# Kernel optimization log

Hardware: AMD Instinct MI355X
Metric: run time of the kernel (lower is better)

Reference implementation:

```python
import jax, jax.numpy as jnp
import numpy as np

N = 100000
E = 1600000
IN_DIM = 128
HID = 64
EPS = 1e-5


def setup_inputs() -> dict:
    key = jax.random.key(0)
    ks = jax.random.split(key, 16)
    x = jax.random.normal(ks[0], (N, IN_DIM), dtype=jnp.float32)
    edge_index = jax.random.randint(ks[1], (2, E), 0, N, dtype=jnp.int32)
    def glorot(k, fan_in, fan_out):
        s = jnp.sqrt(6.0 / (fan_in + fan_out))
        return jax.random.uniform(k, (fan_in, fan_out), jnp.float32, -s, s)
    return {
        "x": x,
        "edge_index": edge_index,
        "W0": glorot(ks[2], IN_DIM, HID), "b0": jnp.zeros((HID,), jnp.float32),
        "W1": glorot(ks[3], HID, HID),    "b1": jnp.zeros((HID,), jnp.float32),
        "W2": glorot(ks[4], HID, HID),    "b2": jnp.zeros((HID,), jnp.float32),
        "g0": jnp.ones((HID,), jnp.float32),  "be0": jnp.zeros((HID,), jnp.float32),
        "g1": jnp.ones((HID,), jnp.float32),  "be1": jnp.zeros((HID,), jnp.float32),
        "g2": jnp.ones((HID,), jnp.float32),  "be2": jnp.zeros((HID,), jnp.float32),
        "fc1_w": glorot(ks[5], HID, 32), "fc1_b": jnp.zeros((32,), jnp.float32),
        "fc2_w": glorot(ks[6], 32, 2),   "fc2_b": jnp.zeros((2,), jnp.float32),
    }


def _gcn_conv(x, src, dst, dis, W, b):
    # x' = D^{-1/2} (A + I) D^{-1/2} (x W) + b ; dis = deg^{-1/2} with self-loops
    h = x @ W                                   # [N, H]
    norm = dis[src] * dis[dst]                  # [E]
    msg = h[src] * norm[:, None]                # [E, H]
    agg = jax.ops.segment_sum(msg, dst, num_segments=N)
    agg = agg + h * (dis * dis)[:, None]        # self-loop contribution
    return agg + b


def _batchnorm(x, gamma, beta):
    mu = jnp.mean(x, axis=0)
    var = jnp.mean(jnp.square(x - mu), axis=0)  # biased, as torch BN training
    return gamma * (x - mu) * jax.lax.rsqrt(var + EPS) + beta


def reference(x, edge_index, W0, b0, W1, b1, W2, b2,
              g0, be0, g1, be1, g2, be2, fc1_w, fc1_b, fc2_w, fc2_b):
    src = edge_index[0]
    dst = edge_index[1]
    deg = jax.ops.segment_sum(jnp.ones((E,), x.dtype), dst, num_segments=N) + 1.0
    dis = jax.lax.rsqrt(deg)                    # deg >= 1 from self-loops
    for W, b, g, be in ((W0, b0, g0, be0), (W1, b1, g1, be1), (W2, b2, g2, be2)):
        x = _gcn_conv(x, src, dst, dis, W, b)
        x = jax.nn.relu(_batchnorm(x, g, be))
        # dropout: identity (deterministic eval)
    x = jax.nn.relu(x @ fc1_w + fc1_b)
    x = x @ fc2_w + fc2_b
    return jax.nn.log_softmax(x, axis=1)
```

## Files before the change

### kernel.cpp

```cpp
#include <hip/hip_runtime.h>
#include <hip/hip_fp16.h>
#include <math.h>


#define BUCK_CAP 6144
#define PB_EDGES 8192

typedef _Float16 f16x8 __attribute__((ext_vector_type(8)));
typedef float f32x4 __attribute__((ext_vector_type(4)));

union H4U { uint2 u; __half h[4]; };
union H8U { uint4 u; __half h[8]; };

__device__ inline uint2 pack4(float a, float b, float c, float d) {
    H4U t;
    t.h[0] = __float2half_rn(a); t.h[1] = __float2half_rn(b);
    t.h[2] = __float2half_rn(c); t.h[3] = __float2half_rn(d);
    return t.u;
}
__device__ inline float4 unpack4(uint2 u) {
    H4U t; t.u = u;
    return make_float4(__half2float(t.h[0]), __half2float(t.h[1]),
                       __half2float(t.h[2]), __half2float(t.h[3]));
}
__device__ inline void upadd8(uint4 u, float* a) {
    H8U t; t.u = u;
#pragma unroll
    for (int i = 0; i < 8; ++i) a[i] += __half2float(t.h[i]);
}

__global__ __launch_bounds__(256) void k_zero(int* __restrict__ gcur,
                                              float* __restrict__ stats) {
    int t = threadIdx.x;
    gcur[t] = 0; gcur[t + 256] = 0;
    stats[t] = 0.f;
    if (t < 128) stats[256 + t] = 0.f;
}

__global__ __launch_bounds__(256) void k_part(const int* __restrict__ src,
                                              const int* __restrict__ dst,
                                              int* __restrict__ gcur,
                                              unsigned* __restrict__ rec,
                                              int E, int NB) {
    __shared__ int hist[512];
    __shared__ int lbase[512];
    __shared__ int gbase[512];
    __shared__ int stmp[256];
    __shared__ unsigned stage[PB_EDGES];
    __shared__ unsigned short sbkt[PB_EDGES];
    const int tid = threadIdx.x;
    const int e0 = blockIdx.x * PB_EDGES;
    const int e1 = min(e0 + PB_EDGES, E);
    const int cnt = e1 - e0;

    hist[tid] = 0; hist[tid + 256] = 0;
    __syncthreads();
    for (int i = e0 + tid; i < e1; i += 256)
        atomicAdd(&hist[dst[i] >> 8], 1);
    __syncthreads();
    for (int b = tid; b < NB; b += 256) {
        int c = hist[b];
        gbase[b] = c ? atomicAdd(&gcur[b], c) : 0;
    }
    int h0 = hist[2 * tid], h1 = hist[2 * tid + 1];
    int psum = h0 + h1;
    stmp[tid] = psum;
    __syncthreads();
    int x = psum;
    for (int off = 1; off < 256; off <<= 1) {
        int y = (tid >= off) ? stmp[tid - off] : 0;
        __syncthreads();
        x += y;
        stmp[tid] = x;
        __syncthreads();
    }
    int excl = x - psum;
    lbase[2 * tid] = excl;
    lbase[2 * tid + 1] = excl + h0;
    __syncthreads();
    hist[2 * tid] = excl;
    hist[2 * tid + 1] = excl + h0;
    __syncthreads();
    for (int i = e0 + tid; i < e1; i += 256) {
        int s = src[i], d = dst[i];
        int b = d >> 8;
        int pos = atomicAdd(&hist[b], 1);
        stage[pos] = ((unsigned)s << 8) | (unsigned)(d & 255);
        sbkt[pos] = (unsigned short)b;
    }
    __syncthreads();
    for (int i = tid; i < cnt; i += 256) {
        int b = sbkt[i];
        rec[(size_t)b * BUCK_CAP + gbase[b] + (i - lbase[b])] = stage[i];
    }
}

__global__ __launch_bounds__(256) void k_bscat(const int* __restrict__ gcur,
                                               const unsigned* __restrict__ rec,
                                               float* __restrict__ dis,
                                               int* __restrict__ row_ptr,
                                               int* __restrict__ ssrc,
                                               int n, int NB, int E) {
    __shared__ int h[256];
    __shared__ int cur[256];
    __shared__ int lb[512];
    __shared__ int stmp[256];
    __shared__ int stage[BUCK_CAP];
    const int b = blockIdx.x, tid = threadIdx.x;
    int g0 = (2 * tid < NB) ? gcur[2 * tid] : 0;
    int g1 = (2 * tid + 1 < NB) ? gcur[2 * tid + 1] : 0;
    int ps = g0 + g1;
    stmp[tid] = ps;
    h[tid] = 0;
    __syncthreads();
    int xx = ps;
    for (int off = 1; off < 256; off <<= 1) {
        int y = (tid >= off) ? stmp[tid - off] : 0;
        __syncthreads();
        xx += y;
        stmp[tid] = xx;
        __syncthreads();
    }
    int ex = xx - ps;
    lb[2 * tid] = ex;
    lb[2 * tid + 1] = ex + g0;
    __syncthreads();
    const int bb = lb[b];
    if (b == 0 && tid == 0) row_ptr[n] = E;

    const int cnt = gcur[b];
    const unsigned* r = rec + (size_t)b * BUCK_CAP;
    for (int i = tid; i < cnt; i += 256)
        atomicAdd(&h[r[i] & 255u], 1);
    __syncthreads();
    const int myd = h[tid];
    const int node = b * 256 + tid;
    if (node < n) dis[node] = rsqrtf((float)myd + 1.0f);
    int x = myd;
    for (int off = 1; off < 256; off <<= 1) {
        int y = (tid >= off) ? h[tid - off] : 0;
        __syncthreads();
        x += y;
        h[tid] = x;
        __syncthreads();
    }
    const int excl = x - myd;
    if (node < n) row_ptr[node] = bb + excl;
    cur[tid] = excl;
    __syncthreads();
    for (int i = tid; i < cnt; i += 256) {
        unsigned v = r[i];
        int pos = atomicAdd(&cur[v & 255u], 1);
        stage[pos] = (int)(v >> 8);
    }
    __syncthreads();
    for (int i = tid; i < cnt; i += 256) ssrc[bb + i] = stage[i];
}

template <int K, bool BN, bool XH>
__global__ __launch_bounds__(256) void k_gemm(const void* __restrict__ Xv,
                                              const float* __restrict__ W,
                                              const float* __restrict__ dis,
                                              const float* __restrict__ stats,
                                              const float* __restrict__ g,
                                              const float* __restrict__ be,
                                              __half* __restrict__ Hp, int n) {
    constexpr int KS = K / 32;
    constexpr int XSTR = K + 8;
    __shared__ __align__(16) __half BF[KS * 4 * 64 * 8];
    __shared__ __align__(16) __half XL[64 * XSTR];
    __shared__ float muS[64], wS[64], bS[64];
    const int tid = threadIdx.x;
    const int row0 = blockIdx.x * 64;

    if constexpr (BN) {
        if (tid < 64) {
            float inv_n = 1.0f / (float)n;
            float m = stats[tid] * inv_n;
            float var = stats[64 + tid] * inv_n - m * m;
            muS[tid] = m;
            wS[tid] = rsqrtf(var + 1e-5f) * g[tid];
            bS[tid] = be[tid];
        }
    }
    for (int i = tid; i < KS * 4 * 64; i += 256) {
        int l = i & 63, fs = i >> 6;
        int ks = fs >> 2, ct = fs & 3;
        int kb = ks * 32 + ((l >> 4) << 3);
        int c = (ct << 4) + (l & 15);
        H8U t;
#pragma unroll
        for (int j = 0; j < 8; ++j) t.h[j] = __float2half_rn(W[(kb + j) * 64 + c]);
        *reinterpret_cast<uint4*>(&BF[i * 8]) = t.u;
    }
    __syncthreads();

    if constexpr (!XH) {
        constexpr int Q4 = K / 4;
        const float4* X4 = (const float4*)Xv;
        for (int it = 0; it < 64 * Q4 / 256; ++it) {
            int idx = it * 256 + tid;
            int row = idx / Q4, q = idx % Q4;
            int grow = row0 + row;
            float4 v = make_float4(0.f, 0.f, 0.f, 0.f);
            if (grow < n) v = X4[(size_t)grow * Q4 + q];
            *reinterpret_cast<uint2*>(&XL[row * XSTR + q * 4]) = pack4(v.x, v.y, v.z, v.w);
        }
    } else {
        constexpr int QU = K / 4;
        const uint2* Xh = (const uint2*)Xv;
        for (int it = 0; it < 64 * QU / 256; ++it) {
            int idx = it * 256 + tid;
            int row = idx / QU, q = idx % QU;
            int grow = row0 + row;
            float4 v = make_float4(0.f, 0.f, 0.f, 0.f);
            if (grow < n) {
                v = unpack4(Xh[(size_t)grow * QU + q]);
                float4 m = *reinterpret_cast<const float4*>(&muS[q * 4]);
                float4 w4 = *reinterpret_cast<const float4*>(&wS[q * 4]);
                float4 b4 = *reinterpret_cast<const float4*>(&bS[q * 4]);
                v.x = fmaxf((v.x - m.x) * w4.x + b4.x, 0.f);
                v.y = fmaxf((v.y - m.y) * w4.y + b4.y, 0.f);
                v.z = fmaxf((v.z - m.z) * w4.z + b4.z, 0.f);
                v.w = fmaxf((v.w - m.w) * w4.w + b4.w, 0.f);
            }
            *reinterpret_cast<uint2*>(&XL[row * XSTR + q * 4]) = pack4(v.x, v.y, v.z, v.w);
        }
    }
    __syncthreads();

    const int wave = tid >> 6, lane = tid & 63;
    const __half* arow = &XL[(wave * 16 + (lane & 15)) * XSTR + ((lane >> 4) << 3)];
    f16x8 a[KS];
#pragma unroll
    for (int ks = 0; ks < KS; ++ks)
        a[ks] = *reinterpret_cast<const f16x8*>(arow + ks * 32);

    f32x4 acc[4];
#pragma unroll
    for (int ct = 0; ct < 4; ++ct) acc[ct] = (f32x4){0.f, 0.f, 0.f, 0.f};
#pragma unroll
    for (int ct = 0; ct < 4; ++ct)
#pragma unroll
        for (int ks = 0; ks < KS; ++ks) {
            f16x8 b = *reinterpret_cast<const f16x8*>(&BF[((ks * 4 + ct) * 64 + lane) * 8]);
            acc[ct] = __builtin_amdgcn_mfma_f32_16x16x32_f16(a[ks], b, acc[ct], 0, 0, 0);
        }

    const int mbase = row0 + wave * 16 + ((lane >> 4) << 2);
#pragma unroll
    for (int reg = 0; reg < 4; ++reg) {
        int grow = mbase + reg;
        if (grow < n) {
            float dd = dis[grow];
#pragma unroll
            for (int ct = 0; ct < 4; ++ct)
                Hp[(size_t)grow * 64 + ct * 16 + (lane & 15)] =
                    __float2half_rn(acc[ct][reg] * dd);
        }
    }
}

__global__ __launch_bounds__(256) void k_gather(const int* __restrict__ row_ptr,
                                                const int* __restrict__ ssrc,
                                                const float* __restrict__ dis,
                                                const uint4* __restrict__ Hp,
                                                uint4* __restrict__ AGG, int n) {
    int t = blockIdx.x * 256 + threadIdx.x;
    int d = t >> 3;
    if (d >= n) return;
    int fi = t & 7;
    int r0 = row_ptr[d], r1 = row_ptr[d + 1];
    float a[8] = {};
    upadd8(Hp[(size_t)d * 8 + fi], a);
    int p = r0;
    for (; p + 7 < r1; p += 8) {
        int s0 = ssrc[p], s1 = ssrc[p + 1], s2 = ssrc[p + 2], s3 = ssrc[p + 3];
        int s4 = ssrc[p + 4], s5 = ssrc[p + 5], s6 = ssrc[p + 6], s7 = ssrc[p + 7];
        uint4 q0 = Hp[(size_t)s0 * 8 + fi];
        uint4 q1 = Hp[(size_t)s1 * 8 + fi];
        uint4 q2 = Hp[(size_t)s2 * 8 + fi];
        uint4 q3 = Hp[(size_t)s3 * 8 + fi];
        uint4 q4 = Hp[(size_t)s4 * 8 + fi];
        uint4 q5 = Hp[(size_t)s5 * 8 + fi];
        uint4 q6 = Hp[(size_t)s6 * 8 + fi];
        uint4 q7 = Hp[(size_t)s7 * 8 + fi];
        upadd8(q0, a); upadd8(q1, a); upadd8(q2, a); upadd8(q3, a);
        upadd8(q4, a); upadd8(q5, a); upadd8(q6, a); upadd8(q7, a);
    }
    for (; p + 3 < r1; p += 4) {
        int s0 = ssrc[p], s1 = ssrc[p + 1], s2 = ssrc[p + 2], s3 = ssrc[p + 3];
        uint4 q0 = Hp[(size_t)s0 * 8 + fi];
        uint4 q1 = Hp[(size_t)s1 * 8 + fi];
        uint4 q2 = Hp[(size_t)s2 * 8 + fi];
        uint4 q3 = Hp[(size_t)s3 * 8 + fi];
        upadd8(q0, a); upadd8(q1, a); upadd8(q2, a); upadd8(q3, a);
    }
    for (; p < r1; ++p) upadd8(Hp[(size_t)ssrc[p] * 8 + fi], a);
    float dd = dis[d];
    H8U o;
#pragma unroll
    for (int i = 0; i < 8; ++i) o.h[i] = __float2half_rn(a[i] * dd);
    AGG[(size_t)d * 8 + fi] = o.u;
}

__global__ __launch_bounds__(256) void k_stats(const uint2* __restrict__ A,
                                               float* __restrict__ stats, int n) {
    __shared__ float r1[16 * 64];
    __shared__ float r2[16 * 64];
    int tid = threadIdx.x;
    int fi = tid & 15, rg = tid >> 4;
    float s0 = 0, s1 = 0, s2 = 0, s3 = 0, q0 = 0, q1 = 0, q2 = 0, q3 = 0;
    for (int row = blockIdx.x * 16 + rg; row < n; row += gridDim.x * 16) {
        float4 v = unpack4(A[(size_t)row * 16 + fi]);
        s0 += v.x; q0 += v.x * v.x;
        s1 += v.y; q1 += v.y * v.y;
        s2 += v.z; q2 += v.z * v.z;
        s3 += v.w; q3 += v.w * v.w;
    }
    r1[rg * 64 + fi * 4 + 0] = s0; r2[rg * 64 + fi * 4 + 0] = q0;
    r1[rg * 64 + fi * 4 + 1] = s1; r2[rg * 64 + fi * 4 + 1] = q1;
    r1[rg * 64 + fi * 4 + 2] = s2; r2[rg * 64 + fi * 4 + 2] = q2;
    r1[rg * 64 + fi * 4 + 3] = s3; r2[rg * 64 + fi * 4 + 3] = q3;
    __syncthreads();
    if (tid < 64) {
        float a = 0;
#pragma unroll
        for (int r = 0; r < 16; ++r) a += r1[r * 64 + tid];
        atomicAdd(&stats[tid], a);
    } else if (tid < 128) {
        int f = tid - 64;
        float a = 0;
#pragma unroll
        for (int r = 0; r < 16; ++r) a += r2[r * 64 + f];
        atomicAdd(&stats[64 + f], a);
    }
}

__global__ __launch_bounds__(256) void k_head(const uint2* __restrict__ X,
                                              const float* __restrict__ stats,
                                              const float* __restrict__ g,
                                              const float* __restrict__ be,
                                              const float* __restrict__ w1,
                                              const float* __restrict__ b1,
                                              const float* __restrict__ w2,
                                              const float* __restrict__ b2,
                                              float* __restrict__ out, int n) {
    __shared__ __align__(16) float w1s[64 * 32];
    __shared__ __align__(16) float b1s[32];
    __shared__ float w2s[64];
    __shared__ float b2s[2];
    __shared__ float muS[64], wS[64], bS[64];
    int tid = threadIdx.x;
    for (int i = tid; i < 512; i += 256)
        reinterpret_cast<float4*>(w1s)[i] = reinterpret_cast<const float4*>(w1)[i];
    if (tid < 32) b1s[tid] = b1[tid];
    if (tid >= 64 && tid < 128) w2s[tid - 64] = w2[tid - 64];
    if (tid >= 128 && tid < 130) b2s[tid - 128] = b2[tid - 128];
    if (tid < 64) {
        float inv_n = 1.0f / (float)n;
        float m = stats[tid] * inv_n;
        float var = stats[64 + tid] * inv_n - m * m;
        muS[tid] = m;
        wS[tid] = rsqrtf(var + 1e-5f) * g[tid];
        bS[tid] = be[tid];
    }
    __syncthreads();
    int row = blockIdx.x * 256 + tid;
    if (row >= n) return;

    float4 h[8];
#pragma unroll
    for (int j4 = 0; j4 < 8; ++j4) h[j4] = reinterpret_cast<float4*>(b1s)[j4];

#pragma unroll
    for (int k4 = 0; k4 < 16; ++k4) {
        float4 xv = unpack4(X[(size_t)row * 16 + k4]);
#pragma unroll
        for (int kk = 0; kk < 4; ++kk) {
            int k = k4 * 4 + kk;
            float raw = (kk == 0) ? xv.x : (kk == 1) ? xv.y : (kk == 2) ? xv.z : xv.w;
            float xk = fmaxf((raw - muS[k]) * wS[k] + bS[k], 0.f);
            const float4* wrow = reinterpret_cast<const float4*>(&w1s[k * 32]);
#pragma unroll
            for (int j4 = 0; j4 < 8; ++j4) {
                float4 wv = wrow[j4];
                h[j4].x += xk * wv.x; h[j4].y += xk * wv.y;
                h[j4].z += xk * wv.z; h[j4].w += xk * wv.w;
            }
        }
    }
    float o0 = b2s[0], o1 = b2s[1];
#pragma unroll
    for (int j4 = 0; j4 < 8; ++j4) {
        float hv[4] = {h[j4].x, h[j4].y, h[j4].z, h[j4].w};
#pragma unroll
        for (int c = 0; c < 4; ++c) {
            float hj = fmaxf(hv[c], 0.f);
            int j = j4 * 4 + c;
            o0 += hj * w2s[2 * j];
            o1 += hj * w2s[2 * j + 1];
        }
    }
    float m = fmaxf(o0, o1);
    float l = __logf(__expf(o0 - m) + __expf(o1 - m));
    reinterpret_cast<float2*>(out)[row] = make_float2(o0 - m - l, o1 - m - l);
}

extern "C" void kernel_launch(void* const* d_in, const int* in_sizes, int n_in,
                              void* d_out, int out_size, void* d_ws, size_t ws_size,
                              hipStream_t stream) {
    const float* x    = (const float*)d_in[0];
    const int*   ei   = (const int*)d_in[1];
    const float* W0   = (const float*)d_in[2];
    const float* W1   = (const float*)d_in[4];
    const float* W2   = (const float*)d_in[6];
    const float* g0   = (const float*)d_in[8];
    const float* be0  = (const float*)d_in[9];
    const float* g1   = (const float*)d_in[10];
    const float* be1  = (const float*)d_in[11];
    const float* g2   = (const float*)d_in[12];
    const float* be2  = (const float*)d_in[13];
    const float* fc1w = (const float*)d_in[14];
    const float* fc1b = (const float*)d_in[15];
    const float* fc2w = (const float*)d_in[16];
    const float* fc2b = (const float*)d_in[17];

    const int N = in_sizes[0] / 128;
    const int E = in_sizes[1] / 2;
    const int* srcp = ei;
    const int* dstp = ei + E;
    const int NB = (N + 255) >> 8;

    char* ws = (char*)d_ws;
    size_t off = 0;
    auto alloc = [&](size_t bytes) -> void* {
        void* p = ws + off;
        off = (off + bytes + 255) & ~(size_t)255;
        return p;
    };
    int*      gcur    = (int*)alloc(512 * 4);
    float*    stats   = (float*)alloc(3 * 128 * 4);
    float*    dis     = (float*)alloc((size_t)N * 4);
    int*      row_ptr = (int*)alloc((size_t)(N + 1) * 4);
    unsigned* rec     = (unsigned*)alloc((size_t)NB * BUCK_CAP * 4);
    int*      ssrc    = (int*)alloc((size_t)E * 4);
    __half*   B0      = (__half*)alloc((size_t)N * 64 * 2);
    __half*   B1      = (__half*)alloc((size_t)N * 64 * 2);

    k_zero<<<1, 256, 0, stream>>>(gcur, stats);
    k_part<<<(E + PB_EDGES - 1) / PB_EDGES, 256, 0, stream>>>(srcp, dstp, gcur, rec, E, NB);
    k_bscat<<<NB, 256, 0, stream>>>(gcur, rec, dis, row_ptr, ssrc, N, NB, E);

    const int gemm_grid = (N + 63) / 64;
    const int gath_grid = (N * 8 + 255) / 256;

    k_gemm<128, false, false><<<gemm_grid, 256, 0, stream>>>(x, W0, dis, nullptr, nullptr, nullptr, B0, N);
    k_gather<<<gath_grid, 256, 0, stream>>>(row_ptr, ssrc, dis, (const uint4*)B0, (uint4*)B1, N);
    k_stats<<<512, 256, 0, stream>>>((const uint2*)B1, stats + 0, N);

    k_gemm<64, true, true><<<gemm_grid, 256, 0, stream>>>(B1, W1, dis, stats + 0, g0, be0, B0, N);
    k_gather<<<gath_grid, 256, 0, stream>>>(row_ptr, ssrc, dis, (const uint4*)B0, (uint4*)B1, N);
    k_stats<<<512, 256, 0, stream>>>((const uint2*)B1, stats + 128, N);

    k_gemm<64, true, true><<<gemm_grid, 256, 0, stream>>>(B1, W2, dis, stats + 128, g1, be1, B0, N);
    k_gather<<<gath_grid, 256, 0, stream>>>(row_ptr, ssrc, dis, (const uint4*)B0, (uint4*)B1, N);
    k_stats<<<512, 256, 0, stream>>>((const uint2*)B1, stats + 256, N);

    k_head<<<(N + 255) / 256, 256, 0, stream>>>((const uint2*)B1, stats + 256, g2, be2,
                                                fc1w, fc1b, fc2w, fc2b,
                                                (float*)d_out, N);
}
```

Baseline: 253.3 us.

## Fuse BatchNorm statistics into gather kernel with striped atomic accumulators

Folds the per-feature sum and sum-of-squares reduction into the gather kernel, which now runs as a fixed grid-stride launch. This drops the separate stats kernel and its re-read of the aggregated half-precision buffer. The stats are computed from fp32 values before fp16 rounding and accumulated into 8 striped slots chosen by block index, which the consumers then sum, to cut atomic contention. The fixed grid of 2048 blocks may lower parallelism and latency hiding in the gather compared with the previous one-thread-per-feature-chunk launch.

```diff
diff --git a/kernel.cpp b/kernel.cpp
--- a/kernel.cpp
+++ b/kernel.cpp
@@ -5,6 +5,7 @@
 
 #define BUCK_CAP 6144
 #define PB_EDGES 8192
+#define GATH_BLOCKS 2048
 
 typedef _Float16 f16x8 __attribute__((ext_vector_type(8)));
 typedef float f32x4 __attribute__((ext_vector_type(4)));
@@ -33,8 +34,8 @@
                                               float* __restrict__ stats) {
     int t = threadIdx.x;
     gcur[t] = 0; gcur[t + 256] = 0;
-    stats[t] = 0.f;
-    if (t < 128) stats[256 + t] = 0.f;
+#pragma unroll
+    for (int k = 0; k < 12; ++k) stats[k * 256 + t] = 0.f;
 }
 
 __global__ __launch_bounds__(256) void k_part(const int* __restrict__ src,
@@ -175,9 +176,15 @@
 
     if constexpr (BN) {
         if (tid < 64) {
+            float s1 = 0.f, s2 = 0.f;
+#pragma unroll
+            for (int r = 0; r < 8; ++r) {
+                s1 += stats[r * 128 + tid];
+                s2 += stats[r * 128 + 64 + tid];
+            }
             float inv_n = 1.0f / (float)n;
-            float m = stats[tid] * inv_n;
-            float var = stats[64 + tid] * inv_n - m * m;
+            float m = s1 * inv_n;
+            float var = s2 * inv_n - m * m;
             muS[tid] = m;
             wS[tid] = rsqrtf(var + 1e-5f) * g[tid];
             bS[tid] = be[tid];
@@ -265,75 +272,69 @@
                                                 const int* __restrict__ ssrc,
                                                 const float* __restrict__ dis,
                                                 const uint4* __restrict__ Hp,
-                                                uint4* __restrict__ AGG, int n) {
-    int t = blockIdx.x * 256 + threadIdx.x;
-    int d = t >> 3;
-    if (d >= n) return;
-    int fi = t & 7;
-    int r0 = row_ptr[d], r1 = row_ptr[d + 1];
-    float a[8] = {};
-    upadd8(Hp[(size_t)d * 8 + fi], a);
-    int p = r0;
-    for (; p + 7 < r1; p += 8) {
-        int s0 = ssrc[p], s1 = ssrc[p + 1], s2 = ssrc[p + 2], s3 = ssrc[p + 3];
-        int s4 = ssrc[p + 4], s5 = ssrc[p + 5], s6 = ssrc[p + 6], s7 = ssrc[p + 7];
-        uint4 q0 = Hp[(size_t)s0 * 8 + fi];
-        uint4 q1 = Hp[(size_t)s1 * 8 + fi];
-        uint4 q2 = Hp[(size_t)s2 * 8 + fi];
-        uint4 q3 = Hp[(size_t)s3 * 8 + fi];
-        uint4 q4 = Hp[(size_t)s4 * 8 + fi];
-        uint4 q5 = Hp[(size_t)s5 * 8 + fi];
-        uint4 q6 = Hp[(size_t)s6 * 8 + fi];
-        uint4 q7 = Hp[(size_t)s7 * 8 + fi];
-        upadd8(q0, a); upadd8(q1, a); upadd8(q2, a); upadd8(q3, a);
-        upadd8(q4, a); upadd8(q5, a); upadd8(q6, a); upadd8(q7, a);
-    }
-    for (; p + 3 < r1; p += 4) {
-        int s0 = ssrc[p], s1 = ssrc[p + 1], s2 = ssrc[p + 2], s3 = ssrc[p + 3];
-        uint4 q0 = Hp[(size_t)s0 * 8 + fi];
-        uint4 q1 = Hp[(size_t)s1 * 8 + fi];
-        uint4 q2 = Hp[(size_t)s2 * 8 + fi];
-        uint4 q3 = Hp[(size_t)s3 * 8 + fi];
-        upadd8(q0, a); upadd8(q1, a); upadd8(q2, a); upadd8(q3, a);
-    }
-    for (; p < r1; ++p) upadd8(Hp[(size_t)ssrc[p] * 8 + fi], a);
-    float dd = dis[d];
-    H8U o;
-#pragma unroll
-    for (int i = 0; i < 8; ++i) o.h[i] = __float2half_rn(a[i] * dd);
-    AGG[(size_t)d * 8 + fi] = o.u;
-}
-
-__global__ __launch_bounds__(256) void k_stats(const uint2* __restrict__ A,
-                                               float* __restrict__ stats, int n) {
-    __shared__ float r1[16 * 64];
-    __shared__ float r2[16 * 64];
-    int tid = threadIdx.x;
-    int fi = tid & 15, rg = tid >> 4;
-    float s0 = 0, s1 = 0, s2 = 0, s3 = 0, q0 = 0, q1 = 0, q2 = 0, q3 = 0;
-    for (int row = blockIdx.x * 16 + rg; row < n; row += gridDim.x * 16) {
-        float4 v = unpack4(A[(size_t)row * 16 + fi]);
-        s0 += v.x; q0 += v.x * v.x;
-        s1 += v.y; q1 += v.y * v.y;
-        s2 += v.z; q2 += v.z * v.z;
-        s3 += v.w; q3 += v.w * v.w;
-    }
-    r1[rg * 64 + fi * 4 + 0] = s0; r2[rg * 64 + fi * 4 + 0] = q0;
-    r1[rg * 64 + fi * 4 + 1] = s1; r2[rg * 64 + fi * 4 + 1] = q1;
-    r1[rg * 64 + fi * 4 + 2] = s2; r2[rg * 64 + fi * 4 + 2] = q2;
-    r1[rg * 64 + fi * 4 + 3] = s3; r2[rg * 64 + fi * 4 + 3] = q3;
+                                                uint4* __restrict__ AGG,
+                                                float* __restrict__ stats, int n) {
+    __shared__ float red[32][64];
+    const int tid = threadIdx.x;
+    const int g = tid >> 3, fi = tid & 7;
+    float sacc[8] = {}, qacc[8] = {};
+    for (int d = blockIdx.x * 32 + g; d < n; d += gridDim.x * 32) {
+        int r0 = row_ptr[d], r1 = row_ptr[d + 1];
+        float a[8] = {};
+        upadd8(Hp[(size_t)d * 8 + fi], a);
+        int p = r0;
+        for (; p + 7 < r1; p += 8) {
+            int s0 = ssrc[p], s1 = ssrc[p + 1], s2 = ssrc[p + 2], s3 = ssrc[p + 3];
+            int s4 = ssrc[p + 4], s5 = ssrc[p + 5], s6 = ssrc[p + 6], s7 = ssrc[p + 7];
+            uint4 q0 = Hp[(size_t)s0 * 8 + fi];
+            uint4 q1 = Hp[(size_t)s1 * 8 + fi];
+            uint4 q2 = Hp[(size_t)s2 * 8 + fi];
+            uint4 q3 = Hp[(size_t)s3 * 8 + fi];
+            uint4 q4 = Hp[(size_t)s4 * 8 + fi];
+            uint4 q5 = Hp[(size_t)s5 * 8 + fi];
+            uint4 q6 = Hp[(size_t)s6 * 8 + fi];
+            uint4 q7 = Hp[(size_t)s7 * 8 + fi];
+            upadd8(q0, a); upadd8(q1, a); upadd8(q2, a); upadd8(q3, a);
+            upadd8(q4, a); upadd8(q5, a); upadd8(q6, a); upadd8(q7, a);
+        }
+        for (; p + 3 < r1; p += 4) {
+            int s0 = ssrc[p], s1 = ssrc[p + 1], s2 = ssrc[p + 2], s3 = ssrc[p + 3];
+            uint4 q0 = Hp[(size_t)s0 * 8 + fi];
+            uint4 q1 = Hp[(size_t)s1 * 8 + fi];
+            uint4 q2 = Hp[(size_t)s2 * 8 + fi];
+            uint4 q3 = Hp[(size_t)s3 * 8 + fi];
+            upadd8(q0, a); upadd8(q1, a); upadd8(q2, a); upadd8(q3, a);
+        }
+        for (; p < r1; ++p) upadd8(Hp[(size_t)ssrc[p] * 8 + fi], a);
+        float dd = dis[d];
+        H8U o;
+#pragma unroll
+        for (int i = 0; i < 8; ++i) {
+            float v = a[i] * dd;
+            o.h[i] = __float2half_rn(v);
+            sacc[i] += v;
+            qacc[i] += v * v;
+        }
+        AGG[(size_t)d * 8 + fi] = o.u;
+    }
+#pragma unroll
+    for (int j = 0; j < 8; ++j) red[g][fi * 8 + j] = sacc[j];
     __syncthreads();
     if (tid < 64) {
-        float a = 0;
-#pragma unroll
-        for (int r = 0; r < 16; ++r) a += r1[r * 64 + tid];
-        atomicAdd(&stats[tid], a);
-    } else if (tid < 128) {
-        int f = tid - 64;
-        float a = 0;
-#pragma unroll
-        for (int r = 0; r < 16; ++r) a += r2[r * 64 + f];
-        atomicAdd(&stats[64 + f], a);
+        float s = 0.f;
+#pragma unroll
+        for (int r = 0; r < 32; ++r) s += red[r][tid];
+        atomicAdd(&stats[(blockIdx.x & 7) * 128 + tid], s);
+    }
+    __syncthreads();
+#pragma unroll
+    for (int j = 0; j < 8; ++j) red[g][fi * 8 + j] = qacc[j];
+    __syncthreads();
+    if (tid < 64) {
+        float s = 0.f;
+#pragma unroll
+        for (int r = 0; r < 32; ++r) s += red[r][tid];
+        atomicAdd(&stats[(blockIdx.x & 7) * 128 + 64 + tid], s);
     }
 }
 
@@ -358,9 +359,15 @@
     if (tid >= 64 && tid < 128) w2s[tid - 64] = w2[tid - 64];
     if (tid >= 128 && tid < 130) b2s[tid - 128] = b2[tid - 128];
     if (tid < 64) {
+        float s1 = 0.f, s2 = 0.f;
+#pragma unroll
+        for (int r = 0; r < 8; ++r) {
+            s1 += stats[r * 128 + tid];
+            s2 += stats[r * 128 + 64 + tid];
+        }
         float inv_n = 1.0f / (float)n;
-        float m = stats[tid] * inv_n;
-        float var = stats[64 + tid] * inv_n - m * m;
+        float m = s1 * inv_n;
+        float var = s2 * inv_n - m * m;
         muS[tid] = m;
         wS[tid] = rsqrtf(var + 1e-5f) * g[tid];
         bS[tid] = be[tid];
@@ -440,7 +447,7 @@
         return p;
     };
     int*      gcur    = (int*)alloc(512 * 4);
-    float*    stats   = (float*)alloc(3 * 128 * 4);
+    float*    stats   = (float*)alloc(3 * 8 * 128 * 4);
     float*    dis     = (float*)alloc((size_t)N * 4);
     int*      row_ptr = (int*)alloc((size_t)(N + 1) * 4);
     unsigned* rec     = (unsigned*)alloc((size_t)NB * BUCK_CAP * 4);
@@ -453,21 +460,17 @@
     k_bscat<<<NB, 256, 0, stream>>>(gcur, rec, dis, row_ptr, ssrc, N, NB, E);
 
     const int gemm_grid = (N + 63) / 64;
-    const int gath_grid = (N * 8 + 255) / 256;
 
     k_gemm<128, false, false><<<gemm_grid, 256, 0, stream>>>(x, W0, dis, nullptr, nullptr, nullptr, B0, N);
-    k_gather<<<gath_grid, 256, 0, stream>>>(row_ptr, ssrc, dis, (const uint4*)B0, (uint4*)B1, N);
-    k_stats<<<512, 256, 0, stream>>>((const uint2*)B1, stats + 0, N);
+    k_gather<<<GATH_BLOCKS, 256, 0, stream>>>(row_ptr, ssrc, dis, (const uint4*)B0, (uint4*)B1, stats + 0, N);
 
     k_gemm<64, true, true><<<gemm_grid, 256, 0, stream>>>(B1, W1, dis, stats + 0, g0, be0, B0, N);
-    k_gather<<<gath_grid, 256, 0, stream>>>(row_ptr, ssrc, dis, (const uint4*)B0, (uint4*)B1, N);
-    k_stats<<<512, 256, 0, stream>>>((const uint2*)B1, stats + 128, N);
-
-    k_gemm<64, true, true><<<gemm_grid, 256, 0, stream>>>(B1, W2, dis, stats + 128, g1, be1, B0, N);
-    k_gather<<<gath_grid, 256, 0, stream>>>(row_ptr, ssrc, dis, (const uint4*)B0, (uint4*)B1, N);
-    k_stats<<<512, 256, 0, stream>>>((const uint2*)B1, stats + 256, N);
-
-    k_head<<<(N + 255) / 256, 256, 0, stream>>>((const uint2*)B1, stats + 256, g2, be2,
+    k_gather<<<GATH_BLOCKS, 256, 0, stream>>>(row_ptr, ssrc, dis, (const uint4*)B0, (uint4*)B1, stats + 1024, N);
+
+    k_gemm<64, true, true><<<gemm_grid, 256, 0, stream>>>(B1, W2, dis, stats + 1024, g1, be1, B0, N);
+    k_gather<<<GATH_BLOCKS, 256, 0, stream>>>(row_ptr, ssrc, dis, (const uint4*)B0, (uint4*)B1, stats + 2048, N);
+
+    k_head<<<(N + 255) / 256, 256, 0, stream>>>((const uint2*)B1, stats + 2048, g2, be2,
                                                 fc1w, fc1b, fc2w, fc2b,
                                                 (float*)d_out, N);
 }
```

After: 218.9 us. -13.6%, faster.
